# Kernel optimization log

Hardware: AMD Instinct MI355X
Metric: run time of the kernel (lower is better)

## Reference

```python
import jax, jax.numpy as jnp
import numpy as np

TEMPERATURE = 0.07


def setup_inputs() -> dict:
    key = jax.random.key(0)
    k1, k2, k3 = jax.random.split(key, 3)
    B, K, D = 256, 512, 1024
    return {
        "bg_img_feature": jax.random.normal(k1, (B, D), dtype=jnp.float32),
        "fg_pro_feature": jax.random.normal(k2, (B, D), dtype=jnp.float32),
        "bg_pro_feature": jax.random.normal(k3, (B, K, D), dtype=jnp.float32),
    }


def reference(bg_img_feature, fg_pro_feature, bg_pro_feature):
    # Normalize only the background image features (as in the torch module).
    bg_img = bg_img_feature / jnp.linalg.norm(bg_img_feature, axis=-1, keepdims=True)
    # Per-sample logits against K background prototypes: [B, K]
    bg_logits = jnp.einsum("bd,bkd->bk", bg_img, bg_pro_feature)
    # Per-sample logit against its own foreground prototype: [B]
    fg_logits = jnp.sum(bg_img * fg_pro_feature, axis=-1)
    inv_t = 1.0 / TEMPERATURE
    # positive_sims = sum_i mean_k exp(bg_logits[i,k] / T)
    pos = jnp.sum(jnp.mean(jnp.exp(bg_logits * inv_t), axis=-1))
    # negative_sims = pos + sum_i exp(fg_logits[i] / T)
    neg = pos + jnp.sum(jnp.exp(fg_logits * inv_t))
    return -jnp.log(pos / neg)
```

## Files before the change

kernel.cpp:

```cpp
#include <hip/hip_runtime.h>
#include <math.h>

#define B_N 256
#define K_N 512
#define D_N 1024
#define INV_T 14.285714285714286


__global__ __launch_bounds__(256) void norm_fg_kernel(
    const float* __restrict__ bg_img, const float* __restrict__ fg_pro,
    double* __restrict__ fgsum, float* __restrict__ inv_norm)
{
  const int b = blockIdx.x;
  const int t = threadIdx.x;
  const float4* a4 = (const float4*)(bg_img + (size_t)b * D_N);
  const float4* f4 = (const float4*)(fg_pro + (size_t)b * D_N);
  float4 a = a4[t];
  float4 f = f4[t];
  float ss = a.x*a.x + a.y*a.y + a.z*a.z + a.w*a.w;
  float fd = a.x*f.x + a.y*f.y + a.z*f.z + a.w*f.w;
  #pragma unroll
  for (int off = 32; off > 0; off >>= 1) {
    ss += __shfl_xor(ss, off);
    fd += __shfl_xor(fd, off);
  }
  __shared__ float sss[4], sfd[4];
  const int wave = t >> 6;
  if ((t & 63) == 0) { sss[wave] = ss; sfd[wave] = fd; }
  __syncthreads();
  if (t == 0) {
    float ssum = (sss[0] + sss[1]) + (sss[2] + sss[3]);
    float fsum = (sfd[0] + sfd[1]) + (sfd[2] + sfd[3]);
    double inv = 1.0 / sqrt((double)ssum);
    inv_norm[b] = (float)inv;
    double fl = (double)fsum * inv * INV_T;
    atomicAdd(fgsum, exp(fl));
  }
}

__global__ __launch_bounds__(256) void dot_exp_kernel(
    const float* __restrict__ bg_img, const float* __restrict__ bg_pro,
    const float* __restrict__ inv_norm, double* __restrict__ pos_part)
{
  const int lane = threadIdx.x & 63;
  const int wib  = threadIdx.x >> 6;
  const int gwave = blockIdx.x * 4 + wib;
  const int p0 = gwave * 4;
  const int b = p0 >> 9;

  const float4* a4 = (const float4*)(bg_img + (size_t)b * D_N);
  const float4 a0 = a4[lane];
  const float4 a1 = a4[lane + 64];
  const float4 a2 = a4[lane + 128];
  const float4 a3 = a4[lane + 192];
  const float inv = inv_norm[b];
  const float invt_f = (float)INV_T;

  double acc = 0.0;
  #pragma unroll
  for (int j = 0; j < 4; ++j) {
    const float4* p4 = (const float4*)(bg_pro + (size_t)(p0 + j) * D_N);
    float4 x0 = p4[lane];
    float4 x1 = p4[lane + 64];
    float4 x2 = p4[lane + 128];
    float4 x3 = p4[lane + 192];
    float s = a0.x*x0.x + a0.y*x0.y + a0.z*x0.z + a0.w*x0.w;
    s += a1.x*x1.x + a1.y*x1.y + a1.z*x1.z + a1.w*x1.w;
    s += a2.x*x2.x + a2.y*x2.y + a2.z*x2.z + a2.w*x2.w;
    s += a3.x*x3.x + a3.y*x3.y + a3.z*x3.z + a3.w*x3.w;
    #pragma unroll
    for (int off = 32; off > 0; off >>= 1) s += __shfl_xor(s, off);
    if (lane == 0) acc += (double)expf(s * inv * invt_f);
  }

  __shared__ double wacc[4];
  if (lane == 0) wacc[wib] = acc;
  __syncthreads();
  if (threadIdx.x == 0) {
    double tsum = (wacc[0] + wacc[1]) + (wacc[2] + wacc[3]);
    atomicAdd(&pos_part[blockIdx.x & 255], tsum);
  }
}

__global__ __launch_bounds__(256) void finalize_kernel(
    const double* __restrict__ pos_part, const double* __restrict__ fgsum,
    float* __restrict__ out)
{
  const int t = threadIdx.x;
  double v = pos_part[t];
  #pragma unroll
  for (int off = 32; off > 0; off >>= 1) v += __shfl_xor(v, off);
  __shared__ double w[4];
  if ((t & 63) == 0) w[t >> 6] = v;
  __syncthreads();
  if (t == 0) {
    double possum = (w[0] + w[1]) + (w[2] + w[3]);
    double pos = possum / (double)K_N;
    double r = *fgsum / pos;
    out[0] = (float)log1p(r);
  }
}

extern "C" void kernel_launch(void* const* d_in, const int* in_sizes, int n_in,
                              void* d_out, int out_size, void* d_ws, size_t ws_size,
                              hipStream_t stream) {
  const float* bg_img = (const float*)d_in[0];
  const float* fg_pro = (const float*)d_in[1];
  const float* bg_pro = (const float*)d_in[2];

  char* ws = (char*)d_ws;
  double* pos_part = (double*)(ws);
  double* fgsum    = (double*)(ws + 2048);
  float*  inv_norm = (float*)(ws + 2112);

  hipMemsetAsync(d_ws, 0, 2056, stream);

  norm_fg_kernel<<<B_N, 256, 0, stream>>>(bg_img, fg_pro, fgsum, inv_norm);

  dot_exp_kernel<<<(B_N * K_N) / 16, 256, 0, stream>>>(bg_img, bg_pro, inv_norm, pos_part);

  finalize_kernel<<<1, 256, 0, stream>>>(pos_part, fgsum, (float*)d_out);
}
```

Measured before the change: 676.9 us.

## Fuse norm and fg computation into dot-exp kernel, drop atomics and memset

The row-norm and foreground dot product move into the main dot-exp kernel, and each wave recomputes the bg_img norm itself. This removes the separate norm kernel, the memset and the double atomics, which are replaced by per-block partial sums that the finalize kernel reduces. All 16 prototype loads are issued up front as nontemporal loads to raise memory-level parallelism for the streamed 512MB tensor. The cost is redundant norm computation in every wave and higher register pressure.

```diff
diff --git a/kernel.cpp b/kernel.cpp
--- a/kernel.cpp
+++ b/kernel.cpp
@@ -6,98 +6,104 @@
 #define D_N 1024
 #define INV_T 14.285714285714286
 
+typedef float vf4 __attribute__((ext_vector_type(4)));
 
-__global__ __launch_bounds__(256) void norm_fg_kernel(
+
+__global__ __launch_bounds__(256) void dot_exp_fused(
     const float* __restrict__ bg_img, const float* __restrict__ fg_pro,
-    double* __restrict__ fgsum, float* __restrict__ inv_norm)
+    const float* __restrict__ bg_pro,
+    double* __restrict__ block_part, double* __restrict__ fg_part)
 {
-  const int b = blockIdx.x;
-  const int t = threadIdx.x;
-  const float4* a4 = (const float4*)(bg_img + (size_t)b * D_N);
-  const float4* f4 = (const float4*)(fg_pro + (size_t)b * D_N);
-  float4 a = a4[t];
-  float4 f = f4[t];
-  float ss = a.x*a.x + a.y*a.y + a.z*a.z + a.w*a.w;
-  float fd = a.x*f.x + a.y*f.y + a.z*f.z + a.w*f.w;
+  const int lane  = threadIdx.x & 63;
+  const int wib   = threadIdx.x >> 6;
+  const int gwave = blockIdx.x * 4 + wib;
+  const int r0    = gwave * 4;
+  const int b     = r0 >> 9;
+
+  const vf4* a4 = (const vf4*)(bg_img + (size_t)b * D_N);
+  const vf4 a0 = a4[lane];
+  const vf4 a1 = a4[lane + 64];
+  const vf4 a2 = a4[lane + 128];
+  const vf4 a3 = a4[lane + 192];
+
+  const vf4* p4 = (const vf4*)(bg_pro + (size_t)r0 * D_N);
+  vf4 x0[4], x1[4], x2[4], x3[4];
+  #pragma unroll
+  for (int j = 0; j < 4; ++j) {
+    const vf4* r = p4 + j * 256;
+    x0[j] = __builtin_nontemporal_load(r + lane);
+    x1[j] = __builtin_nontemporal_load(r + lane + 64);
+    x2[j] = __builtin_nontemporal_load(r + lane + 128);
+    x3[j] = __builtin_nontemporal_load(r + lane + 192);
+  }
+
+  float ss;
+  {
+    vf4 m = a0 * a0 + a1 * a1 + a2 * a2 + a3 * a3;
+    ss = (m.x + m.y) + (m.z + m.w);
+  }
+
+  float s[4];
+  #pragma unroll
+  for (int j = 0; j < 4; ++j) {
+    vf4 m = a0 * x0[j] + a1 * x1[j] + a2 * x2[j] + a3 * x3[j];
+    s[j] = (m.x + m.y) + (m.z + m.w);
+  }
+
   #pragma unroll
   for (int off = 32; off > 0; off >>= 1) {
-    ss += __shfl_xor(ss, off);
-    fd += __shfl_xor(fd, off);
+    ss   += __shfl_xor(ss,   off);
+    s[0] += __shfl_xor(s[0], off);
+    s[1] += __shfl_xor(s[1], off);
+    s[2] += __shfl_xor(s[2], off);
+    s[3] += __shfl_xor(s[3], off);
   }
-  __shared__ float sss[4], sfd[4];
-  const int wave = t >> 6;
-  if ((t & 63) == 0) { sss[wave] = ss; sfd[wave] = fd; }
-  __syncthreads();
-  if (t == 0) {
-    float ssum = (sss[0] + sss[1]) + (sss[2] + sss[3]);
-    float fsum = (sfd[0] + sfd[1]) + (sfd[2] + sfd[3]);
-    double inv = 1.0 / sqrt((double)ssum);
-    inv_norm[b] = (float)inv;
-    double fl = (double)fsum * inv * INV_T;
-    atomicAdd(fgsum, exp(fl));
-  }
-}
 
-__global__ __launch_bounds__(256) void dot_exp_kernel(
-    const float* __restrict__ bg_img, const float* __restrict__ bg_pro,
-    const float* __restrict__ inv_norm, double* __restrict__ pos_part)
-{
-  const int lane = threadIdx.x & 63;
-  const int wib  = threadIdx.x >> 6;
-  const int gwave = blockIdx.x * 4 + wib;
-  const int p0 = gwave * 4;
-  const int b = p0 >> 9;
+  const double inv   = 1.0 / sqrt((double)ss);
+  const float  scale = (float)(inv * INV_T);
 
-  const float4* a4 = (const float4*)(bg_img + (size_t)b * D_N);
-  const float4 a0 = a4[lane];
-  const float4 a1 = a4[lane + 64];
-  const float4 a2 = a4[lane + 128];
-  const float4 a3 = a4[lane + 192];
-  const float inv = inv_norm[b];
-  const float invt_f = (float)INV_T;
+  const double e = (double)expf(s[0] * scale) + (double)expf(s[1] * scale)
+                 + (double)expf(s[2] * scale) + (double)expf(s[3] * scale);
 
-  double acc = 0.0;
-  #pragma unroll
-  for (int j = 0; j < 4; ++j) {
-    const float4* p4 = (const float4*)(bg_pro + (size_t)(p0 + j) * D_N);
-    float4 x0 = p4[lane];
-    float4 x1 = p4[lane + 64];
-    float4 x2 = p4[lane + 128];
-    float4 x3 = p4[lane + 192];
-    float s = a0.x*x0.x + a0.y*x0.y + a0.z*x0.z + a0.w*x0.w;
-    s += a1.x*x1.x + a1.y*x1.y + a1.z*x1.z + a1.w*x1.w;
-    s += a2.x*x2.x + a2.y*x2.y + a2.z*x2.z + a2.w*x2.w;
-    s += a3.x*x3.x + a3.y*x3.y + a3.z*x3.z + a3.w*x3.w;
+  if ((r0 & (K_N - 1)) == 0) {
+    const vf4* f4 = (const vf4*)(fg_pro + (size_t)b * D_N);
+    vf4 m = a0 * f4[lane] + a1 * f4[lane + 64]
+          + a2 * f4[lane + 128] + a3 * f4[lane + 192];
+    float fs = (m.x + m.y) + (m.z + m.w);
     #pragma unroll
-    for (int off = 32; off > 0; off >>= 1) s += __shfl_xor(s, off);
-    if (lane == 0) acc += (double)expf(s * inv * invt_f);
+    for (int off = 32; off > 0; off >>= 1) fs += __shfl_xor(fs, off);
+    if (lane == 0) fg_part[b] = exp((double)fs * inv * INV_T);
   }
 
   __shared__ double wacc[4];
-  if (lane == 0) wacc[wib] = acc;
+  if (lane == 0) wacc[wib] = e;
   __syncthreads();
-  if (threadIdx.x == 0) {
-    double tsum = (wacc[0] + wacc[1]) + (wacc[2] + wacc[3]);
-    atomicAdd(&pos_part[blockIdx.x & 255], tsum);
-  }
+  if (threadIdx.x == 0)
+    block_part[blockIdx.x] = (wacc[0] + wacc[1]) + (wacc[2] + wacc[3]);
 }
 
 __global__ __launch_bounds__(256) void finalize_kernel(
-    const double* __restrict__ pos_part, const double* __restrict__ fgsum,
+    const double* __restrict__ block_part, const double* __restrict__ fg_part,
     float* __restrict__ out)
 {
   const int t = threadIdx.x;
-  double v = pos_part[t];
+  double v = 0.0;
   #pragma unroll
-  for (int off = 32; off > 0; off >>= 1) v += __shfl_xor(v, off);
-  __shared__ double w[4];
-  if ((t & 63) == 0) w[t >> 6] = v;
+  for (int i = 0; i < 32; ++i) v += block_part[t + 256 * i];
+  double f = fg_part[t];
+  #pragma unroll
+  for (int off = 32; off > 0; off >>= 1) {
+    v += __shfl_xor(v, off);
+    f += __shfl_xor(f, off);
+  }
+  __shared__ double wv[4], wf[4];
+  const int w = t >> 6;
+  if ((t & 63) == 0) { wv[w] = v; wf[w] = f; }
   __syncthreads();
   if (t == 0) {
-    double possum = (w[0] + w[1]) + (w[2] + w[3]);
-    double pos = possum / (double)K_N;
-    double r = *fgsum / pos;
-    out[0] = (float)log1p(r);
+    double pos = ((wv[0] + wv[1]) + (wv[2] + wv[3])) / (double)K_N;
+    double fg  = (wf[0] + wf[1]) + (wf[2] + wf[3]);
+    out[0] = (float)log1p(fg / pos);
   }
 }
 
@@ -109,15 +115,10 @@
   const float* bg_pro = (const float*)d_in[2];
 
   char* ws = (char*)d_ws;
-  double* pos_part = (double*)(ws);
-  double* fgsum    = (double*)(ws + 2048);
-  float*  inv_norm = (float*)(ws + 2112);
+  double* block_part = (double*)(ws);
+  double* fg_part    = (double*)(ws + 65536);
 
-  hipMemsetAsync(d_ws, 0, 2056, stream);
-
-  norm_fg_kernel<<<B_N, 256, 0, stream>>>(bg_img, fg_pro, fgsum, inv_norm);
-
-  dot_exp_kernel<<<(B_N * K_N) / 16, 256, 0, stream>>>(bg_img, bg_pro, inv_norm, pos_part);
-
-  finalize_kernel<<<1, 256, 0, stream>>>(pos_part, fgsum, (float*)d_out);
+  dot_exp_fused<<<(B_N * K_N) / 16, 256, 0, stream>>>(
+      bg_img, fg_pro, bg_pro, block_part, fg_part);
+  finalize_kernel<<<1, 256, 0, stream>>>(block_part, fg_part, (float*)d_out);
 }
```

Result: faster. 647.1 us (-4.4%).
